# Performance work log

Hardware: AMD Instinct MI355X
Metric: run time of the kernel (lower is better)

## Reference

```python
import jax, jax.numpy as jnp
import numpy as np

N_NODES = 50000
N_EDGES = 800000
IN_DIM = 256
HID = 64


def _gcn_conv(x, src, dst, W, b, num_nodes):
    # PyG GCNConv: h = D^{-1/2} (A + I) D^{-1/2} (x @ W) + b
    h = x @ W  # [N, out]
    loop = jnp.arange(num_nodes)
    s = jnp.concatenate([src, loop])  # add self-loops
    d = jnp.concatenate([dst, loop])
    deg = jax.ops.segment_sum(jnp.ones_like(s, dtype=h.dtype), d, num_segments=num_nodes)
    dinv = jnp.where(deg > 0, deg ** -0.5, 0.0)
    norm = dinv[s] * dinv[d]  # [E+N]
    msgs = h[s] * norm[:, None]  # gather + scale
    out = jax.ops.segment_sum(msgs, d, num_segments=num_nodes)  # scatter-add to dst
    return out + b


def setup_inputs() -> dict:
    key = jax.random.key(0)
    ks = jax.random.split(key, 8)
    x = jax.random.normal(ks[0], (N_NODES, IN_DIM), dtype=jnp.float32)
    edge_index = jax.random.randint(ks[1], (2, N_EDGES), 0, N_NODES, dtype=jnp.int64)
    # Glorot-ish init for weights
    W1 = jax.random.normal(ks[2], (IN_DIM, HID), dtype=jnp.float32) * (1.0 / np.sqrt(IN_DIM))
    b1 = jnp.zeros((HID,), dtype=jnp.float32)
    W2 = jax.random.normal(ks[3], (HID, HID), dtype=jnp.float32) * (1.0 / np.sqrt(HID))
    b2 = jnp.zeros((HID,), dtype=jnp.float32)
    Wc = jax.random.normal(ks[4], (HID, 1), dtype=jnp.float32) * (1.0 / np.sqrt(HID))
    bc = jnp.zeros((1,), dtype=jnp.float32)
    return {"x": x, "edge_index": edge_index, "W1": W1, "b1": b1, "W2": W2, "b2": b2, "Wc": Wc, "bc": bc}


def reference(x, edge_index, W1, b1, W2, b2, Wc, bc):
    num_nodes = x.shape[0]
    src, dst = edge_index[0], edge_index[1]
    h = jax.nn.relu(_gcn_conv(x, src, dst, W1, b1, num_nodes))
    h = jax.nn.relu(_gcn_conv(h, src, dst, W2, b2, num_nodes))
    return jax.nn.sigmoid(h @ Wc + bc)  # [N, 1]
```

## Files before the change

### kernel.cpp

```cpp
#include <hip/hip_runtime.h>
#include <math.h>

#define N_NODES 50000
#define N_EDGES 800000
#define IN_DIM 256
#define HID 64
#define BKT 256
#define NBKT ((N_NODES + BKT - 1) / BKT)
#define CAP 8192
#define CHUNK 4096
#define NCH ((N_EDGES + CHUNK - 1) / CHUNK)
#define NGB ((N_NODES + 63) / 64)

typedef short short8v __attribute__((ext_vector_type(8)));
typedef float f32x4 __attribute__((ext_vector_type(4)));
typedef unsigned uint4v __attribute__((ext_vector_type(4)));

__device__ __forceinline__ unsigned short f2bf(float f) {
  unsigned u = __builtin_bit_cast(unsigned, f);
  u += 0x7FFFu + ((u >> 16) & 1u);
  return (unsigned short)(u >> 16);
}
__device__ __forceinline__ unsigned pack2(float a, float b) {
  return (unsigned)f2bf(a) | ((unsigned)f2bf(b) << 16);
}
__device__ __forceinline__ float bfu_lo(unsigned u) {
  return __builtin_bit_cast(float, u << 16);
}
__device__ __forceinline__ float bfu_hi(unsigned u) {
  return __builtin_bit_cast(float, u & 0xFFFF0000u);
}

__global__ void k_prep(int* __restrict__ bcur, const float* __restrict__ W1,
                       const float* __restrict__ W2, unsigned short* __restrict__ Wt1,
                       unsigned short* __restrict__ Wt2) {
  const int t = threadIdx.x;
  if (blockIdx.x == 0) {
    bcur[t] = 0;
  } else if (blockIdx.x == 1) {
    for (int j = 0; j < 64; ++j) {
      int lin = j * 256 + t;
      int k = lin >> 6, c = lin & 63;
      Wt1[c * 256 + k] = f2bf(W1[lin]);
    }
  } else {
    for (int j = 0; j < 16; ++j) {
      int lin = j * 256 + t;
      int k = lin >> 6, c = lin & 63;
      Wt2[c * 64 + k] = f2bf(W2[lin]);
    }
  }
}

__global__ __launch_bounds__(256) void k_g1split(
    const float* __restrict__ X, const unsigned short* __restrict__ Wt1g,
    unsigned short* __restrict__ outA, const int* __restrict__ src,
    const int* __restrict__ dst, int* __restrict__ bcur, unsigned* __restrict__ ebuf) {
  const int t = threadIdx.x;
  if (blockIdx.x < NGB) {
    const int lane = t & 63, wv = t >> 6;
    const int row0 = blockIdx.x * 64;
    int r = row0 + wv * 16 + (lane & 15);
    if (r > N_NODES - 1) r = N_NODES - 1;
    const int kh = (lane >> 4) * 8;

    f32x4 acc[4] = {};
#pragma unroll
    for (int k0 = 0; k0 < IN_DIM; k0 += 32) {
      const float* Xp = X + (size_t)r * IN_DIM + k0 + kh;
      const float4 x0 = *reinterpret_cast<const float4*>(Xp);
      const float4 x1 = *reinterpret_cast<const float4*>(Xp + 4);
      uint4v p;
      p.x = pack2(x0.x, x0.y); p.y = pack2(x0.z, x0.w);
      p.z = pack2(x1.x, x1.y); p.w = pack2(x1.z, x1.w);
      short8v a = __builtin_bit_cast(short8v, p);
#pragma unroll
      for (int n = 0; n < 4; ++n) {
        short8v b = *reinterpret_cast<const short8v*>(
            Wt1g + (size_t)(n * 16 + (lane & 15)) * IN_DIM + k0 + kh);
        acc[n] = __builtin_amdgcn_mfma_f32_16x16x32_bf16(a, b, acc[n], 0, 0, 0);
      }
    }
    const int r0 = row0 + wv * 16;
#pragma unroll
    for (int j = 0; j < 4; ++j) {
      int rr = r0 + (lane >> 4) * 4 + j;
      if (rr < N_NODES) {
#pragma unroll
        for (int n = 0; n < 4; ++n)
          outA[(size_t)rr * 64 + n * 16 + (lane & 15)] = f2bf(acc[n][j]);
      }
    }
  } else {
    __shared__ int cnt[NBKT];
    __shared__ int cur[NBKT];
    for (int i = t; i < NBKT; i += 256) cnt[i] = 0;
    __syncthreads();
    const int base = (blockIdx.x - NGB) * CHUNK;
#pragma unroll
    for (int i = 0; i < CHUNK / 256; ++i) {
      int e = base + i * 256 + t;
      if (e < N_EDGES) atomicAdd(&cnt[dst[e] >> 8], 1);
    }
    __syncthreads();
    for (int i = t; i < NBKT; i += 256) {
      int c = cnt[i];
      cur[i] = c ? (i * CAP + atomicAdd(&bcur[i], c)) : 0;
    }
    __syncthreads();
#pragma unroll
    for (int i = 0; i < CHUNK / 256; ++i) {
      int e = base + i * 256 + t;
      if (e < N_EDGES) {
        int d = dst[e];
        int p = atomicAdd(&cur[d >> 8], 1);
        ebuf[p] = ((unsigned)src[e] << 8) | (unsigned)(d & 255);
      }
    }
  }
}

__global__ void k_bucket(const unsigned* __restrict__ ebuf, const int* __restrict__ bcur,
                         int* __restrict__ rowptr, int* __restrict__ colidx,
                         float* __restrict__ dinv) {
  __shared__ int sA[256];
  __shared__ int sB[256];
  const int b = blockIdx.x, t = threadIdx.x;

  sA[t] = (t < NBKT) ? bcur[t] : 0;
  __syncthreads();
  for (int d = 1; d < 256; d <<= 1) {
    int v = sA[t];
    int a = (t >= d) ? sA[t - d] : 0;
    __syncthreads();
    sA[t] = v + a;
    __syncthreads();
  }
  const int prefix = (b == 0) ? 0 : sA[b - 1];
  const int cntb = bcur[b];
  const int sbeg = b * CAP, send = sbeg + cntb;
  __syncthreads();

  sA[t] = 0;
  __syncthreads();
  for (int i = sbeg + t; i < send; i += 256) atomicAdd(&sA[ebuf[i] & 255], 1);
  __syncthreads();
  const int myc = sA[t];
  sB[t] = myc;
  __syncthreads();
  for (int d = 1; d < 256; d <<= 1) {
    int v = sB[t];
    int a = (t >= d) ? sB[t - d] : 0;
    __syncthreads();
    sB[t] = v + a;
    __syncthreads();
  }
  const int node = b * BKT + t;
  const int ex = prefix + sB[t] - myc;
  if (node < N_NODES) {
    rowptr[node] = ex;
    dinv[node] = rsqrtf((float)(myc + 1));
    if (node == N_NODES - 1) rowptr[N_NODES] = N_EDGES;
  }
  __syncthreads();
  sB[t] = ex;
  __syncthreads();
  for (int i = sbeg + t; i < send; i += 256) {
    unsigned p = ebuf[i];
    int pos = atomicAdd(&sB[p & 255], 1);
    colidx[pos] = (int)(p >> 8);
  }
}

__global__ __launch_bounds__(256) void k_edinv(const int* __restrict__ colidx,
                                               const float* __restrict__ dinv,
                                               float* __restrict__ dinvE) {
  int i = (blockIdx.x * 256 + threadIdx.x) * 4;
  if (i < N_EDGES) {
    int4 c = *reinterpret_cast<const int4*>(&colidx[i]);
    float4 o;
    o.x = dinv[c.x]; o.y = dinv[c.y]; o.z = dinv[c.z]; o.w = dinv[c.w];
    *reinterpret_cast<float4*>(&dinvE[i]) = o;
  }
}

__global__ __launch_bounds__(256) void k_agg_gemm(
    const unsigned short* __restrict__ h, const int* __restrict__ rowptr,
    const int* __restrict__ col, const float* __restrict__ dinv,
    const float* __restrict__ dinvE, const float* __restrict__ bias,
    const unsigned short* __restrict__ Wt2g, unsigned short* __restrict__ out) {
  const int t = threadIdx.x, lane = t & 63, wv = t >> 6;
  const int g = lane >> 3, f0 = (lane & 7) * 8;
  const int vbase = blockIdx.x * 32;
  const int v = vbase + wv * 8 + g;
  const int lrow = wv * 8 + g;

  __shared__ unsigned short h1s[32][72];

  if (v < N_NODES) {
    int e = rowptr[v];
    const int end = rowptr[v + 1];
    const float sv = dinv[v];

    uint4 sw = *reinterpret_cast<const uint4*>(&h[(size_t)v * 64 + f0]);
    float acc0 = sv * bfu_lo(sw.x), acc1 = sv * bfu_hi(sw.x);
    float acc2 = sv * bfu_lo(sw.y), acc3 = sv * bfu_hi(sw.y);
    float acc4 = sv * bfu_lo(sw.z), acc5 = sv * bfu_hi(sw.z);
    float acc6 = sv * bfu_lo(sw.w), acc7 = sv * bfu_hi(sw.w);

#define EDGE1(cc, dv)                                                         \
  {                                                                           \
    uint4 w = *reinterpret_cast<const uint4*>(&h[(size_t)(cc) * 64 + f0]);    \
    acc0 = fmaf(dv, bfu_lo(w.x), acc0); acc1 = fmaf(dv, bfu_hi(w.x), acc1);   \
    acc2 = fmaf(dv, bfu_lo(w.y), acc2); acc3 = fmaf(dv, bfu_hi(w.y), acc3);   \
    acc4 = fmaf(dv, bfu_lo(w.z), acc4); acc5 = fmaf(dv, bfu_hi(w.z), acc5);   \
    acc6 = fmaf(dv, bfu_lo(w.w), acc6); acc7 = fmaf(dv, bfu_hi(w.w), acc7);   \
  }
    while (e < end && (e & 3)) { EDGE1(col[e], dinvE[e]); ++e; }
    for (; e + 4 <= end; e += 4) {
      int4 cc = *reinterpret_cast<const int4*>(&col[e]);
      float4 dd = *reinterpret_cast<const float4*>(&dinvE[e]);
      EDGE1(cc.x, dd.x);
      EDGE1(cc.y, dd.y);
      EDGE1(cc.z, dd.z);
      EDGE1(cc.w, dd.w);
    }
    for (; e < end; ++e) { EDGE1(col[e], dinvE[e]); }
#undef EDGE1

    const float4 ba = *reinterpret_cast<const float4*>(&bias[f0]);
    const float4 bb = *reinterpret_cast<const float4*>(&bias[f0 + 4]);
    float v0 = fmaxf(fmaf(sv, acc0, ba.x), 0.0f);
    float v1 = fmaxf(fmaf(sv, acc1, ba.y), 0.0f);
    float v2 = fmaxf(fmaf(sv, acc2, ba.z), 0.0f);
    float v3 = fmaxf(fmaf(sv, acc3, ba.w), 0.0f);
    float v4 = fmaxf(fmaf(sv, acc4, bb.x), 0.0f);
    float v5 = fmaxf(fmaf(sv, acc5, bb.y), 0.0f);
    float v6 = fmaxf(fmaf(sv, acc6, bb.z), 0.0f);
    float v7 = fmaxf(fmaf(sv, acc7, bb.w), 0.0f);

    uint4 o;
    o.x = pack2(v0, v1); o.y = pack2(v2, v3);
    o.z = pack2(v4, v5); o.w = pack2(v6, v7);
    *reinterpret_cast<uint4*>(&h1s[lrow][f0]) = o;
  } else {
    uint4 z = {0, 0, 0, 0};
    *reinterpret_cast<uint4*>(&h1s[lrow][f0]) = z;
  }
  __syncthreads();

  const int kh = (lane >> 4) * 8;
  f32x4 acc2r[2] = {};
#pragma unroll
  for (int rt = 0; rt < 2; ++rt) {
#pragma unroll
    for (int k0 = 0; k0 < 64; k0 += 32) {
      short8v a = *reinterpret_cast<const short8v*>(&h1s[rt * 16 + (lane & 15)][k0 + kh]);
      short8v b = *reinterpret_cast<const short8v*>(
          Wt2g + (size_t)(wv * 16 + (lane & 15)) * 64 + k0 + kh);
      acc2r[rt] = __builtin_amdgcn_mfma_f32_16x16x32_bf16(a, b, acc2r[rt], 0, 0, 0);
    }
  }
#pragma unroll
  for (int rt = 0; rt < 2; ++rt) {
#pragma unroll
    for (int j = 0; j < 4; ++j) {
      int vg = vbase + rt * 16 + (lane >> 4) * 4 + j;
      if (vg < N_NODES)
        out[(size_t)vg * 64 + wv * 16 + (lane & 15)] = f2bf(acc2r[rt][j] * dinv[vg]);
    }
  }
}

__global__ __launch_bounds__(256) void k_agg_fin(
    const unsigned short* __restrict__ h, const int* __restrict__ rowptr,
    const int* __restrict__ col, const float* __restrict__ dinv,
    const float* __restrict__ bias, const float* __restrict__ Wc,
    const float* __restrict__ bc, float* __restrict__ out) {
  const int t = threadIdx.x, lane = t & 63;
  const int g = lane >> 3, f0 = (lane & 7) * 8;
  const int v = blockIdx.x * 32 + (t >> 6) * 8 + g;
  if (v >= N_NODES) return;

  int e = rowptr[v];
  const int end = rowptr[v + 1];

  uint4 sw = *reinterpret_cast<const uint4*>(&h[(size_t)v * 64 + f0]);
  float acc0 = bfu_lo(sw.x), acc1 = bfu_hi(sw.x);
  float acc2 = bfu_lo(sw.y), acc3 = bfu_hi(sw.y);
  float acc4 = bfu_lo(sw.z), acc5 = bfu_hi(sw.z);
  float acc6 = bfu_lo(sw.w), acc7 = bfu_hi(sw.w);

#define EDGE2(cc)                                                           \
  {                                                                         \
    uint4 w = *reinterpret_cast<const uint4*>(&h[(size_t)(cc) * 64 + f0]);  \
    acc0 += bfu_lo(w.x); acc1 += bfu_hi(w.x);                               \
    acc2 += bfu_lo(w.y); acc3 += bfu_hi(w.y);                               \
    acc4 += bfu_lo(w.z); acc5 += bfu_hi(w.z);                               \
    acc6 += bfu_lo(w.w); acc7 += bfu_hi(w.w);                               \
  }
  while (e < end && (e & 3)) { EDGE2(col[e]); ++e; }
  for (; e + 4 <= end; e += 4) {
    int4 cc = *reinterpret_cast<const int4*>(&col[e]);
    EDGE2(cc.x);
    EDGE2(cc.y);
    EDGE2(cc.z);
    EDGE2(cc.w);
  }
  for (; e < end; ++e) { EDGE2(col[e]); }
#undef EDGE2

  const float sv = dinv[v];
  const float4 ba = *reinterpret_cast<const float4*>(&bias[f0]);
  const float4 bb = *reinterpret_cast<const float4*>(&bias[f0 + 4]);
  const float4 wa = *reinterpret_cast<const float4*>(&Wc[f0]);
  const float4 wb = *reinterpret_cast<const float4*>(&Wc[f0 + 4]);
  float p = fmaxf(fmaf(sv, acc0, ba.x), 0.0f) * wa.x +
            fmaxf(fmaf(sv, acc1, ba.y), 0.0f) * wa.y +
            fmaxf(fmaf(sv, acc2, ba.z), 0.0f) * wa.z +
            fmaxf(fmaf(sv, acc3, ba.w), 0.0f) * wa.w +
            fmaxf(fmaf(sv, acc4, bb.x), 0.0f) * wb.x +
            fmaxf(fmaf(sv, acc5, bb.y), 0.0f) * wb.y +
            fmaxf(fmaf(sv, acc6, bb.z), 0.0f) * wb.z +
            fmaxf(fmaf(sv, acc7, bb.w), 0.0f) * wb.w;
  p += __shfl_xor(p, 1);
  p += __shfl_xor(p, 2);
  p += __shfl_xor(p, 4);
  if ((lane & 7) == 0) out[v] = 1.0f / (1.0f + expf(-(p + bc[0])));
}

extern "C" void kernel_launch(void* const* d_in, const int* in_sizes, int n_in,
                              void* d_out, int out_size, void* d_ws, size_t ws_size,
                              hipStream_t stream) {
  const float* x  = (const float*)d_in[0];
  const int*   ei = (const int*)d_in[1];
  const float* W1 = (const float*)d_in[2];
  const float* b1 = (const float*)d_in[3];
  const float* W2 = (const float*)d_in[4];
  const float* b2 = (const float*)d_in[5];
  const float* Wc = (const float*)d_in[6];
  const float* bc = (const float*)d_in[7];
  float* out = (float*)d_out;

  const int* src = ei;
  const int* dst = ei + N_EDGES;

  unsigned* w = (unsigned*)d_ws;
  int*   bcur   = (int*)(w + 0);
  int*   rowptr = (int*)(w + 256);
  int*   colidx = (int*)(w + 50688);
  unsigned* ebuf = w + 850688;
  float* dinv   = (float*)(w + 2456320);
  float* dinvE  = (float*)(w + 2506496);
  unsigned short* Wt1g = (unsigned short*)(w + 3306496);
  unsigned short* Wt2g = (unsigned short*)(w + 3314688);
  unsigned short* A_bf = (unsigned short*)(w + 3316736);
  unsigned short* B_bf = (unsigned short*)(w + 4916736);

  k_prep<<<3, 256, 0, stream>>>(bcur, W1, W2, Wt1g, Wt2g);
  k_g1split<<<NGB + NCH, 256, 0, stream>>>(x, Wt1g, A_bf, src, dst, bcur, ebuf);
  k_bucket<<<NBKT, 256, 0, stream>>>(ebuf, bcur, rowptr, colidx, dinv);
  k_edinv<<<(N_EDGES / 4 + 255) / 256, 256, 0, stream>>>(colidx, dinv, dinvE);

  const int NAB = (N_NODES + 31) / 32;
  k_agg_gemm<<<NAB, 256, 0, stream>>>(A_bf, rowptr, colidx, dinv, dinvE, b1, Wt2g, B_bf);
  k_agg_fin<<<NAB, 256, 0, stream>>>(B_bf, rowptr, colidx, dinv, b2, Wc, bc, out);
}
```

Before: 104.7 us.

## Split GEMM1 from edge bucketing and stage bucketed edges in LDS before writing

Separates the combined GEMM/edge-split kernel into two launches. The split kernel now sorts each chunk's edges by bucket in shared memory with a local prefix scan, then writes them out contiguously per bucket, replacing scattered global writes. The bucket id is packed into the top byte of each entry, and k_bucket masks it off. The new GEMM1 kernel stages W1 in LDS and preloads all X fragments before running the MFMAs. This costs an extra launch, and the two phases no longer overlap within one grid.

Result: no change. 106.1 us (+1.3%).

```diff
diff --git a/kernel.cpp b/kernel.cpp
--- a/kernel.cpp
+++ b/kernel.cpp
@@ -52,71 +52,59 @@
   }
 }
 
-__global__ __launch_bounds__(256) void k_g1split(
-    const float* __restrict__ X, const unsigned short* __restrict__ Wt1g,
-    unsigned short* __restrict__ outA, const int* __restrict__ src,
-    const int* __restrict__ dst, int* __restrict__ bcur, unsigned* __restrict__ ebuf) {
+__global__ __launch_bounds__(256) void k_split(const int* __restrict__ src,
+                                               const int* __restrict__ dst,
+                                               int* __restrict__ bcur,
+                                               unsigned* __restrict__ ebuf) {
+  __shared__ unsigned stage[CHUNK];
+  __shared__ int cnt[256];
+  __shared__ int off[256];
+  __shared__ int gbase[256];
+  __shared__ int lcur[256];
   const int t = threadIdx.x;
-  if (blockIdx.x < NGB) {
-    const int lane = t & 63, wv = t >> 6;
-    const int row0 = blockIdx.x * 64;
-    int r = row0 + wv * 16 + (lane & 15);
-    if (r > N_NODES - 1) r = N_NODES - 1;
-    const int kh = (lane >> 4) * 8;
-
-    f32x4 acc[4] = {};
-#pragma unroll
-    for (int k0 = 0; k0 < IN_DIM; k0 += 32) {
-      const float* Xp = X + (size_t)r * IN_DIM + k0 + kh;
-      const float4 x0 = *reinterpret_cast<const float4*>(Xp);
-      const float4 x1 = *reinterpret_cast<const float4*>(Xp + 4);
-      uint4v p;
-      p.x = pack2(x0.x, x0.y); p.y = pack2(x0.z, x0.w);
-      p.z = pack2(x1.x, x1.y); p.w = pack2(x1.z, x1.w);
-      short8v a = __builtin_bit_cast(short8v, p);
-#pragma unroll
-      for (int n = 0; n < 4; ++n) {
-        short8v b = *reinterpret_cast<const short8v*>(
-            Wt1g + (size_t)(n * 16 + (lane & 15)) * IN_DIM + k0 + kh);
-        acc[n] = __builtin_amdgcn_mfma_f32_16x16x32_bf16(a, b, acc[n], 0, 0, 0);
-      }
-    }
-    const int r0 = row0 + wv * 16;
-#pragma unroll
-    for (int j = 0; j < 4; ++j) {
-      int rr = r0 + (lane >> 4) * 4 + j;
-      if (rr < N_NODES) {
-#pragma unroll
-        for (int n = 0; n < 4; ++n)
-          outA[(size_t)rr * 64 + n * 16 + (lane & 15)] = f2bf(acc[n][j]);
-      }
-    }
-  } else {
-    __shared__ int cnt[NBKT];
-    __shared__ int cur[NBKT];
-    for (int i = t; i < NBKT; i += 256) cnt[i] = 0;
+  const int base = blockIdx.x * CHUNK;
+  const int valid = min(CHUNK, N_EDGES - base);
+
+  cnt[t] = 0;
+  __syncthreads();
+#pragma unroll
+  for (int i = 0; i < CHUNK / 256; ++i) {
+    int e = base + i * 256 + t;
+    if (e < N_EDGES) atomicAdd(&cnt[dst[e] >> 8], 1);
+  }
+  __syncthreads();
+  {
+    int c = cnt[t];
+    off[t] = c;
     __syncthreads();
-    const int base = (blockIdx.x - NGB) * CHUNK;
-#pragma unroll
-    for (int i = 0; i < CHUNK / 256; ++i) {
-      int e = base + i * 256 + t;
-      if (e < N_EDGES) atomicAdd(&cnt[dst[e] >> 8], 1);
-    }
-    __syncthreads();
-    for (int i = t; i < NBKT; i += 256) {
-      int c = cnt[i];
-      cur[i] = c ? (i * CAP + atomicAdd(&bcur[i], c)) : 0;
-    }
-    __syncthreads();
-#pragma unroll
-    for (int i = 0; i < CHUNK / 256; ++i) {
-      int e = base + i * 256 + t;
-      if (e < N_EDGES) {
-        int d = dst[e];
-        int p = atomicAdd(&cur[d >> 8], 1);
-        ebuf[p] = ((unsigned)src[e] << 8) | (unsigned)(d & 255);
-      }
-    }
+    for (int d = 1; d < 256; d <<= 1) {
+      int v = off[t];
+      int a = (t >= d) ? off[t - d] : 0;
+      __syncthreads();
+      off[t] = v + a;
+      __syncthreads();
+    }
+    int ex = off[t] - c;
+    off[t] = ex;
+    lcur[t] = ex;
+    gbase[t] = (t < NBKT && c) ? (t * CAP + atomicAdd(&bcur[t], c)) : 0;
+  }
+  __syncthreads();
+#pragma unroll
+  for (int i = 0; i < CHUNK / 256; ++i) {
+    int e = base + i * 256 + t;
+    if (e < N_EDGES) {
+      int d = dst[e];
+      int b = d >> 8;
+      int p = atomicAdd(&lcur[b], 1);
+      stage[p] = ((unsigned)b << 24) | ((unsigned)src[e] << 8) | (unsigned)(d & 255);
+    }
+  }
+  __syncthreads();
+  for (int i = t; i < valid; i += 256) {
+    unsigned u = stage[i];
+    int b = u >> 24;
+    ebuf[gbase[b] + (i - off[b])] = u;
   }
 }
 
@@ -168,7 +156,7 @@
   for (int i = sbeg + t; i < send; i += 256) {
     unsigned p = ebuf[i];
     int pos = atomicAdd(&sB[p & 255], 1);
-    colidx[pos] = (int)(p >> 8);
+    colidx[pos] = (int)((p >> 8) & 0xFFFFu);
   }
 }
 
@@ -181,6 +169,61 @@
     float4 o;
     o.x = dinv[c.x]; o.y = dinv[c.y]; o.z = dinv[c.z]; o.w = dinv[c.w];
     *reinterpret_cast<float4*>(&dinvE[i]) = o;
+  }
+}
+
+__global__ __launch_bounds__(256) void k_gemm1(const float* __restrict__ X,
+                                               const unsigned short* __restrict__ Wt1g,
+                                               unsigned short* __restrict__ outA) {
+  __shared__ unsigned short Wl[64][IN_DIM + 8];
+  const int t = threadIdx.x, lane = t & 63, wv = t >> 6;
+
+#pragma unroll
+  for (int j = 0; j < 8; ++j) {
+    int grp = j * 256 + t;
+    int r = grp >> 5, c = (grp & 31) * 8;
+    *reinterpret_cast<short8v*>(&Wl[r][c]) =
+        *reinterpret_cast<const short8v*>(&Wt1g[r * IN_DIM + c]);
+  }
+
+  const int row0 = blockIdx.x * 64;
+  int r = row0 + wv * 16 + (lane & 15);
+  if (r > N_NODES - 1) r = N_NODES - 1;
+  const int kh = (lane >> 4) * 8;
+
+  uint4v ap[8];
+#pragma unroll
+  for (int k0 = 0; k0 < 8; ++k0) {
+    const float* Xp = X + (size_t)r * IN_DIM + k0 * 32 + kh;
+    const float4 x0 = *reinterpret_cast<const float4*>(Xp);
+    const float4 x1 = *reinterpret_cast<const float4*>(Xp + 4);
+    uint4v p;
+    p.x = pack2(x0.x, x0.y); p.y = pack2(x0.z, x0.w);
+    p.z = pack2(x1.x, x1.y); p.w = pack2(x1.z, x1.w);
+    ap[k0] = p;
+  }
+  __syncthreads();
+
+  f32x4 acc[4] = {};
+#pragma unroll
+  for (int k0 = 0; k0 < 8; ++k0) {
+    short8v a = __builtin_bit_cast(short8v, ap[k0]);
+#pragma unroll
+    for (int n = 0; n < 4; ++n) {
+      short8v b = *reinterpret_cast<const short8v*>(&Wl[n * 16 + (lane & 15)][k0 * 32 + kh]);
+      acc[n] = __builtin_amdgcn_mfma_f32_16x16x32_bf16(a, b, acc[n], 0, 0, 0);
+    }
+  }
+
+  const int r0 = row0 + wv * 16;
+#pragma unroll
+  for (int j = 0; j < 4; ++j) {
+    int rr = r0 + (lane >> 4) * 4 + j;
+    if (rr < N_NODES) {
+#pragma unroll
+      for (int n = 0; n < 4; ++n)
+        outA[(size_t)rr * 64 + n * 16 + (lane & 15)] = f2bf(acc[n][j]);
+    }
   }
 }
 
@@ -358,7 +401,8 @@
   unsigned short* B_bf = (unsigned short*)(w + 4916736);
 
   k_prep<<<3, 256, 0, stream>>>(bcur, W1, W2, Wt1g, Wt2g);
-  k_g1split<<<NGB + NCH, 256, 0, stream>>>(x, Wt1g, A_bf, src, dst, bcur, ebuf);
+  k_split<<<NCH, 256, 0, stream>>>(src, dst, bcur, ebuf);
+  k_gemm1<<<NGB, 256, 0, stream>>>(x, Wt1g, A_bf);
   k_bucket<<<NBKT, 256, 0, stream>>>(ebuf, bcur, rowptr, colidx, dinv);
   k_edinv<<<(N_EDGES / 4 + 255) / 256, 256, 0, stream>>>(colidx, dinv, dinvE);
 
```

## Prescale layer-1 features by dinv in bucket kernel, drop per-edge dinv array

Applied to the files above, without the earlier changes.

Folds the source-side D^{-1/2} scaling of the first GCN layer into the bucket kernel, which rescales each node's bf16 feature row in place. The first aggregation then becomes a plain sum, so the k_edinv kernel and its 800k-entry dinvE array go away. This removes one launch and the per-edge dinv gather and read. The gather loop is also unrolled by 8, and the first GEMM now stages W1 in LDS. In exchange the stored features are rounded to bf16 a second time, and the scaling pass adds an extra read-modify-write of the feature buffer.

New measurement: 100.7 us. 1.04x faster.

```diff
diff --git a/kernel.cpp b/kernel.cpp
--- a/kernel.cpp
+++ b/kernel.cpp
@@ -56,31 +56,48 @@
     const float* __restrict__ X, const unsigned short* __restrict__ Wt1g,
     unsigned short* __restrict__ outA, const int* __restrict__ src,
     const int* __restrict__ dst, int* __restrict__ bcur, unsigned* __restrict__ ebuf) {
+  __shared__ unsigned short Wl[64][IN_DIM + 8];
+  __shared__ int cnt[NBKT];
+  __shared__ int cur[NBKT];
   const int t = threadIdx.x;
   if (blockIdx.x < NGB) {
     const int lane = t & 63, wv = t >> 6;
+#pragma unroll
+    for (int j = 0; j < 8; ++j) {
+      int grp = j * 256 + t;
+      int r = grp >> 5, c = (grp & 31) * 8;
+      *reinterpret_cast<short8v*>(&Wl[r][c]) =
+          *reinterpret_cast<const short8v*>(&Wt1g[r * IN_DIM + c]);
+    }
     const int row0 = blockIdx.x * 64;
     int r = row0 + wv * 16 + (lane & 15);
     if (r > N_NODES - 1) r = N_NODES - 1;
     const int kh = (lane >> 4) * 8;
 
-    f32x4 acc[4] = {};
-#pragma unroll
-    for (int k0 = 0; k0 < IN_DIM; k0 += 32) {
-      const float* Xp = X + (size_t)r * IN_DIM + k0 + kh;
+    uint4v ap[8];
+#pragma unroll
+    for (int k0 = 0; k0 < 8; ++k0) {
+      const float* Xp = X + (size_t)r * IN_DIM + k0 * 32 + kh;
       const float4 x0 = *reinterpret_cast<const float4*>(Xp);
       const float4 x1 = *reinterpret_cast<const float4*>(Xp + 4);
       uint4v p;
       p.x = pack2(x0.x, x0.y); p.y = pack2(x0.z, x0.w);
       p.z = pack2(x1.x, x1.y); p.w = pack2(x1.z, x1.w);
-      short8v a = __builtin_bit_cast(short8v, p);
+      ap[k0] = p;
+    }
+    __syncthreads();
+
+    f32x4 acc[4] = {};
+#pragma unroll
+    for (int k0 = 0; k0 < 8; ++k0) {
+      short8v a = __builtin_bit_cast(short8v, ap[k0]);
 #pragma unroll
       for (int n = 0; n < 4; ++n) {
-        short8v b = *reinterpret_cast<const short8v*>(
-            Wt1g + (size_t)(n * 16 + (lane & 15)) * IN_DIM + k0 + kh);
+        short8v b = *reinterpret_cast<const short8v*>(&Wl[n * 16 + (lane & 15)][k0 * 32 + kh]);
         acc[n] = __builtin_amdgcn_mfma_f32_16x16x32_bf16(a, b, acc[n], 0, 0, 0);
       }
     }
+
     const int r0 = row0 + wv * 16;
 #pragma unroll
     for (int j = 0; j < 4; ++j) {
@@ -92,8 +109,6 @@
       }
     }
   } else {
-    __shared__ int cnt[NBKT];
-    __shared__ int cur[NBKT];
     for (int i = t; i < NBKT; i += 256) cnt[i] = 0;
     __syncthreads();
     const int base = (blockIdx.x - NGB) * CHUNK;
@@ -122,9 +137,10 @@
 
 __global__ void k_bucket(const unsigned* __restrict__ ebuf, const int* __restrict__ bcur,
                          int* __restrict__ rowptr, int* __restrict__ colidx,
-                         float* __restrict__ dinv) {
+                         float* __restrict__ dinv, unsigned short* __restrict__ hbuf) {
   __shared__ int sA[256];
   __shared__ int sB[256];
+  __shared__ float sD[256];
   const int b = blockIdx.x, t = threadIdx.x;
 
   sA[t] = (t < NBKT) ? bcur[t] : 0;
@@ -156,10 +172,13 @@
     __syncthreads();
   }
   const int node = b * BKT + t;
+  const bool valid = node < N_NODES;
   const int ex = prefix + sB[t] - myc;
-  if (node < N_NODES) {
+  const float dv = rsqrtf((float)(myc + 1));
+  sD[t] = dv;
+  if (valid) {
     rowptr[node] = ex;
-    dinv[node] = rsqrtf((float)(myc + 1));
+    dinv[node] = dv;
     if (node == N_NODES - 1) rowptr[N_NODES] = N_EDGES;
   }
   __syncthreads();
@@ -170,25 +189,61 @@
     int pos = atomicAdd(&sB[p & 255], 1);
     colidx[pos] = (int)(p >> 8);
   }
-}
-
-__global__ __launch_bounds__(256) void k_edinv(const int* __restrict__ colidx,
-                                               const float* __restrict__ dinv,
-                                               float* __restrict__ dinvE) {
-  int i = (blockIdx.x * 256 + threadIdx.x) * 4;
-  if (i < N_EDGES) {
-    int4 c = *reinterpret_cast<const int4*>(&colidx[i]);
-    float4 o;
-    o.x = dinv[c.x]; o.y = dinv[c.y]; o.z = dinv[c.z]; o.w = dinv[c.w];
-    *reinterpret_cast<float4*>(&dinvE[i]) = o;
-  }
-}
+
+  const int rsub = t >> 3, f8 = (t & 7) * 8;
+#pragma unroll
+  for (int g = 0; g < 8; ++g) {
+    int lr = g * 32 + rsub;
+    int nd = b * BKT + lr;
+    if (nd < N_NODES) {
+      float s = sD[lr];
+      unsigned short* hp = &hbuf[(size_t)nd * 64 + f8];
+      uint4 hv = *reinterpret_cast<const uint4*>(hp);
+      uint4 o;
+      o.x = pack2(s * bfu_lo(hv.x), s * bfu_hi(hv.x));
+      o.y = pack2(s * bfu_lo(hv.y), s * bfu_hi(hv.y));
+      o.z = pack2(s * bfu_lo(hv.z), s * bfu_hi(hv.z));
+      o.w = pack2(s * bfu_lo(hv.w), s * bfu_hi(hv.w));
+      *reinterpret_cast<uint4*>(hp) = o;
+    }
+  }
+}
+
+#define EDGEP(hbuf, cc)                                                       \
+  {                                                                           \
+    uint4 w = *reinterpret_cast<const uint4*>(&hbuf[(size_t)(cc) * 64 + f0]); \
+    acc0 += bfu_lo(w.x); acc1 += bfu_hi(w.x);                                 \
+    acc2 += bfu_lo(w.y); acc3 += bfu_hi(w.y);                                 \
+    acc4 += bfu_lo(w.z); acc5 += bfu_hi(w.z);                                 \
+    acc6 += bfu_lo(w.w); acc7 += bfu_hi(w.w);                                 \
+  }
+
+#define GATHER_PLAIN(hbuf, EV, ENDV)                                               \
+  uint4 sw = *reinterpret_cast<const uint4*>(&hbuf[(size_t)v * 64 + f0]);          \
+  float acc0 = bfu_lo(sw.x), acc1 = bfu_hi(sw.x);                                  \
+  float acc2 = bfu_lo(sw.y), acc3 = bfu_hi(sw.y);                                  \
+  float acc4 = bfu_lo(sw.z), acc5 = bfu_hi(sw.z);                                  \
+  float acc6 = bfu_lo(sw.w), acc7 = bfu_hi(sw.w);                                  \
+  int e = EV;                                                                      \
+  const int end = ENDV;                                                            \
+  while (e < end && (e & 3)) { EDGEP(hbuf, col[e]); ++e; }                         \
+  for (; e + 8 <= end; e += 8) {                                                   \
+    int4 ca = *reinterpret_cast<const int4*>(&col[e]);                             \
+    int4 cb = *reinterpret_cast<const int4*>(&col[e + 4]);                         \
+    EDGEP(hbuf, ca.x); EDGEP(hbuf, ca.y); EDGEP(hbuf, ca.z); EDGEP(hbuf, ca.w);    \
+    EDGEP(hbuf, cb.x); EDGEP(hbuf, cb.y); EDGEP(hbuf, cb.z); EDGEP(hbuf, cb.w);    \
+  }                                                                                \
+  for (; e + 4 <= end; e += 4) {                                                   \
+    int4 cc = *reinterpret_cast<const int4*>(&col[e]);                             \
+    EDGEP(hbuf, cc.x); EDGEP(hbuf, cc.y); EDGEP(hbuf, cc.z); EDGEP(hbuf, cc.w);    \
+  }                                                                                \
+  for (; e < end; ++e) { EDGEP(hbuf, col[e]); }
 
 __global__ __launch_bounds__(256) void k_agg_gemm(
     const unsigned short* __restrict__ h, const int* __restrict__ rowptr,
     const int* __restrict__ col, const float* __restrict__ dinv,
-    const float* __restrict__ dinvE, const float* __restrict__ bias,
-    const unsigned short* __restrict__ Wt2g, unsigned short* __restrict__ out) {
+    const float* __restrict__ bias, const unsigned short* __restrict__ Wt2g,
+    unsigned short* __restrict__ out) {
   const int t = threadIdx.x, lane = t & 63, wv = t >> 6;
   const int g = lane >> 3, f0 = (lane & 7) * 8;
   const int vbase = blockIdx.x * 32;
@@ -198,35 +253,8 @@
   __shared__ unsigned short h1s[32][72];
 
   if (v < N_NODES) {
-    int e = rowptr[v];
-    const int end = rowptr[v + 1];
     const float sv = dinv[v];
-
-    uint4 sw = *reinterpret_cast<const uint4*>(&h[(size_t)v * 64 + f0]);
-    float acc0 = sv * bfu_lo(sw.x), acc1 = sv * bfu_hi(sw.x);
-    float acc2 = sv * bfu_lo(sw.y), acc3 = sv * bfu_hi(sw.y);
-    float acc4 = sv * bfu_lo(sw.z), acc5 = sv * bfu_hi(sw.z);
-    float acc6 = sv * bfu_lo(sw.w), acc7 = sv * bfu_hi(sw.w);
-
-#define EDGE1(cc, dv)                                                         \
-  {                                                                           \
-    uint4 w = *reinterpret_cast<const uint4*>(&h[(size_t)(cc) * 64 + f0]);    \
-    acc0 = fmaf(dv, bfu_lo(w.x), acc0); acc1 = fmaf(dv, bfu_hi(w.x), acc1);   \
-    acc2 = fmaf(dv, bfu_lo(w.y), acc2); acc3 = fmaf(dv, bfu_hi(w.y), acc3);   \
-    acc4 = fmaf(dv, bfu_lo(w.z), acc4); acc5 = fmaf(dv, bfu_hi(w.z), acc5);   \
-    acc6 = fmaf(dv, bfu_lo(w.w), acc6); acc7 = fmaf(dv, bfu_hi(w.w), acc7);   \
-  }
-    while (e < end && (e & 3)) { EDGE1(col[e], dinvE[e]); ++e; }
-    for (; e + 4 <= end; e += 4) {
-      int4 cc = *reinterpret_cast<const int4*>(&col[e]);
-      float4 dd = *reinterpret_cast<const float4*>(&dinvE[e]);
-      EDGE1(cc.x, dd.x);
-      EDGE1(cc.y, dd.y);
-      EDGE1(cc.z, dd.z);
-      EDGE1(cc.w, dd.w);
-    }
-    for (; e < end; ++e) { EDGE1(col[e], dinvE[e]); }
-#undef EDGE1
+    GATHER_PLAIN(h, rowptr[v], rowptr[v + 1])
 
     const float4 ba = *reinterpret_cast<const float4*>(&bias[f0]);
     const float4 bb = *reinterpret_cast<const float4*>(&bias[f0 + 4]);
@@ -282,33 +310,7 @@
   const int v = blockIdx.x * 32 + (t >> 6) * 8 + g;
   if (v >= N_NODES) return;
 
-  int e = rowptr[v];
-  const int end = rowptr[v + 1];
-
-  uint4 sw = *reinterpret_cast<const uint4*>(&h[(size_t)v * 64 + f0]);
-  float acc0 = bfu_lo(sw.x), acc1 = bfu_hi(sw.x);
-  float acc2 = bfu_lo(sw.y), acc3 = bfu_hi(sw.y);
-  float acc4 = bfu_lo(sw.z), acc5 = bfu_hi(sw.z);
-  float acc6 = bfu_lo(sw.w), acc7 = bfu_hi(sw.w);
-
-#define EDGE2(cc)                                                           \
-  {                                                                         \
-    uint4 w = *reinterpret_cast<const uint4*>(&h[(size_t)(cc) * 64 + f0]);  \
-    acc0 += bfu_lo(w.x); acc1 += bfu_hi(w.x);                               \
-    acc2 += bfu_lo(w.y); acc3 += bfu_hi(w.y);                               \
-    acc4 += bfu_lo(w.z); acc5 += bfu_hi(w.z);                               \
-    acc6 += bfu_lo(w.w); acc7 += bfu_hi(w.w);                               \
-  }
-  while (e < end && (e & 3)) { EDGE2(col[e]); ++e; }
-  for (; e + 4 <= end; e += 4) {
-    int4 cc = *reinterpret_cast<const int4*>(&col[e]);
-    EDGE2(cc.x);
-    EDGE2(cc.y);
-    EDGE2(cc.z);
-    EDGE2(cc.w);
-  }
-  for (; e < end; ++e) { EDGE2(col[e]); }
-#undef EDGE2
+  GATHER_PLAIN(h, rowptr[v], rowptr[v + 1])
 
   const float sv = dinv[v];
   const float4 ba = *reinterpret_cast<const float4*>(&bias[f0]);
@@ -351,18 +353,16 @@
   int*   colidx = (int*)(w + 50688);
   unsigned* ebuf = w + 850688;
   float* dinv   = (float*)(w + 2456320);
-  float* dinvE  = (float*)(w + 2506496);
-  unsigned short* Wt1g = (unsigned short*)(w + 3306496);
-  unsigned short* Wt2g = (unsigned short*)(w + 3314688);
-  unsigned short* A_bf = (unsigned short*)(w + 3316736);
-  unsigned short* B_bf = (unsigned short*)(w + 4916736);
+  unsigned short* Wt1g = (unsigned short*)(w + 2506496);
+  unsigned short* Wt2g = (unsigned short*)(w + 2514688);
+  unsigned short* A_bf = (unsigned short*)(w + 2516736);
+  unsigned short* B_bf = (unsigned short*)(w + 4116736);
 
   k_prep<<<3, 256, 0, stream>>>(bcur, W1, W2, Wt1g, Wt2g);
   k_g1split<<<NGB + NCH, 256, 0, stream>>>(x, Wt1g, A_bf, src, dst, bcur, ebuf);
-  k_bucket<<<NBKT, 256, 0, stream>>>(ebuf, bcur, rowptr, colidx, dinv);
-  k_edinv<<<(N_EDGES / 4 + 255) / 256, 256, 0, stream>>>(colidx, dinv, dinvE);
+  k_bucket<<<NBKT, 256, 0, stream>>>(ebuf, bcur, rowptr, colidx, dinv, A_bf);
 
   const int NAB = (N_NODES + 31) / 32;
-  k_agg_gemm<<<NAB, 256, 0, stream>>>(A_bf, rowptr, colidx, dinv, dinvE, b1, Wt2g, B_bf);
+  k_agg_gemm<<<NAB, 256, 0, stream>>>(A_bf, rowptr, colidx, dinv, b1, Wt2g, B_bf);
   k_agg_fin<<<NAB, 256, 0, stream>>>(B_bf, rowptr, colidx, dinv, b2, Wc, bc, out);
 }
```
